# Performance work log

Measured on AMD Instinct MI355X. Metric: run time of the kernel, lower is better.

## Reference

```python
import jax, jax.numpy as jnp
import numpy as np

NUM_USERS = 100000
NUM_ITEMS = 50000
N_NODES = NUM_USERS + NUM_ITEMS
N_EDGES = 3200000
EMB_DIM = 128
N_LAYERS = 3


def setup_inputs() -> dict:
    key = jax.random.key(0)
    ks = jax.random.split(key, 7)
    # nn.init.normal_(std=0.1) embedding init
    user_emb = jax.random.normal(ks[0], (NUM_USERS, EMB_DIM), dtype=jnp.float32) * 0.1
    item_emb = jax.random.normal(ks[1], (NUM_ITEMS, EMB_DIM), dtype=jnp.float32) * 0.1
    # static normalized adjacency in COO form (values from D^-1/2 A D^-1/2 are positive)
    edge_row = jax.random.randint(ks[2], (N_EDGES,), 0, N_NODES, dtype=jnp.int32)
    edge_col = jax.random.randint(ks[3], (N_EDGES,), 0, N_NODES, dtype=jnp.int32)
    edge_val = jax.random.uniform(ks[4], (N_EDGES,), dtype=jnp.float32)
    users = jax.random.randint(ks[5], (2048,), 0, NUM_USERS, dtype=jnp.int32)
    items = jax.random.randint(ks[6], (2048,), 0, NUM_ITEMS, dtype=jnp.int32)
    return {
        "user_emb": user_emb,
        "item_emb": item_emb,
        "edge_val": edge_val,
        "edge_row": edge_row,
        "edge_col": edge_col,
        "users": users,
        "items": items,
    }


def reference(user_emb, item_emb, edge_val, edge_row, edge_col, users, items):
    # computer(): concat user/item tables -> [N, d]
    all_emb = jnp.concatenate([user_emb, item_emb], axis=0)
    acc = all_emb  # running sum of layer embeddings (fused mean over layers)
    emb = all_emb
    for _ in range(N_LAYERS):
        # sparse.mm(G, emb): per-edge gather, scale, scatter-add
        msg = edge_val[:, None] * emb[edge_col]  # [E, d]
        emb = jax.ops.segment_sum(msg, edge_row, num_segments=N_NODES)
        acc = acc + emb
    light_out = acc / jnp.float32(N_LAYERS + 1)  # mean over stacked layer embeddings
    users_emb = light_out[users]
    items_emb = light_out[NUM_USERS + items]
    # gamma = sum(users_emb * items_emb, dim=1)
    return jnp.sum(users_emb * items_emb, axis=1)
```

## Files before the change

kernel.cpp:

```cpp
#include <hip/hip_runtime.h>

#define D 128
#define NUSERS 100000
#define NITEMS 50000
#define NNODES 150000
#define NEDGES 3200000
#define NSEL 2048
#define NBKT 586
#define PBLK 1024
#define EPB (NEDGES / PBLK)
#define MATN (NBKT * PBLK)
#define MB (MATN / 256)
#define BCAP 8192
#define INIT_BLKS 2048
#define FLG_BLKS ((NNODES + 255) / 256)
#define SELSET_BLKS ((2 * NSEL + 255) / 256)
#define COLMASK 0x3FFFFu

typedef unsigned int uint_t;
typedef unsigned short ushort_t;

__device__ inline uint_t bf16_rne(float f) {
    uint_t x = __float_as_uint(f);
    return (x + 0x7FFFu + ((x >> 16) & 1u)) >> 16;
}

__device__ inline int block_excl_scan(int v, int* lds, int nw) {
    int lane = threadIdx.x & 63;
    int wid = (int)(threadIdx.x >> 6);
    int x = v;
    #pragma unroll
    for (int off = 1; off < 64; off <<= 1) {
        int y = __shfl_up(x, off);
        if (lane >= off) x += y;
    }
    if (lane == 63) lds[wid] = x;
    __syncthreads();
    if (wid == 0) {
        int s = (lane < nw) ? lds[lane] : 0;
        #pragma unroll
        for (int off = 1; off < 16; off <<= 1) {
            int y = __shfl_up(s, off);
            if (lane >= off) s += y;
        }
        if (lane < nw) lds[lane] = s;
    }
    __syncthreads();
    int waveoff = (wid == 0) ? 0 : lds[wid - 1];
    return waveoff + x - v;
}

__global__ void k_prologue(const int* __restrict__ row, int* __restrict__ mat,
                           const float4* __restrict__ u4, const float4* __restrict__ i4,
                           uint4* __restrict__ cur,
                           int* __restrict__ flags, int* __restrict__ selflag) {
    __shared__ int h[NBKT];
    int blk = blockIdx.x;
    if (blk < PBLK) {
        for (int i = threadIdx.x; i < NBKT; i += 256) h[i] = 0;
        __syncthreads();
        int beg = blk * EPB, end = beg + EPB;
        for (int e = beg + threadIdx.x; e < end; e += 256)
            atomicAdd(&h[row[e] >> 8], 1);
        __syncthreads();
        for (int i = threadIdx.x; i < NBKT; i += 256)
            mat[i * PBLK + blk] = h[i];
    } else if (blk < PBLK + INIT_BLKS) {
        size_t total8 = (size_t)NNODES * D / 8;
        size_t ub8 = (size_t)NUSERS * D / 8;
        size_t stride = (size_t)INIT_BLKS * 256;
        for (size_t i = (size_t)(blk - PBLK) * 256 + threadIdx.x; i < total8; i += stride) {
            const float4* src = (i < ub8) ? &u4[2 * i] : &i4[2 * (i - ub8)];
            float4 a = src[0], b = src[1];
            uint4 o;
            o.x = (bf16_rne(a.y) << 16) | bf16_rne(a.x);
            o.y = (bf16_rne(a.w) << 16) | bf16_rne(a.z);
            o.z = (bf16_rne(b.y) << 16) | bf16_rne(b.x);
            o.w = (bf16_rne(b.w) << 16) | bf16_rne(b.z);
            cur[i] = o;
        }
    } else {
        int i = (blk - PBLK - INIT_BLKS) * 256 + threadIdx.x;
        if (i < NNODES) { flags[i] = 0; selflag[i] = 0; }
    }
}

__global__ void k_blocksum(const int* __restrict__ src, int* __restrict__ bsums, int n) {
    int i = blockIdx.x * 256 + threadIdx.x;
    int v = (i < n) ? src[i] : 0;
    #pragma unroll
    for (int off = 32; off; off >>= 1) v += __shfl_down(v, off);
    __shared__ int lds[4];
    int lane = threadIdx.x & 63, wid = (int)(threadIdx.x >> 6);
    if (lane == 0) lds[wid] = v;
    __syncthreads();
    if (threadIdx.x == 0) bsums[blockIdx.x] = lds[0] + lds[1] + lds[2] + lds[3];
}

__global__ void k_scan2(int* __restrict__ mat, const int* __restrict__ bsums, int n,
                        const int* __restrict__ users, const int* __restrict__ items,
                        int* __restrict__ selflag, int* __restrict__ flags) {
    int b = blockIdx.x;
    if (b >= MB) {
        int idx = (b - MB) * 256 + threadIdx.x;
        if (idx < 2 * NSEL) {
            int node = (idx < NSEL) ? users[idx] : NUSERS + items[idx - NSEL];
            selflag[node] = 1;
            flags[node] = 1;
        }
        return;
    }
    __shared__ int red[4];
    __shared__ int lds[4];
    int lane = threadIdx.x & 63, wid = (int)(threadIdx.x >> 6);
    int s = 0;
    for (int j = threadIdx.x; j < b; j += 256) s += bsums[j];
    #pragma unroll
    for (int off = 32; off; off >>= 1) s += __shfl_down(s, off);
    if (lane == 0) red[wid] = s;
    __syncthreads();
    int base = red[0] + red[1] + red[2] + red[3];
    int i = b * 256 + threadIdx.x;
    int v = (i < n) ? mat[i] : 0;
    int ex = block_excl_scan(v, lds, 4);
    if (i < n) mat[i] = base + ex;
}

__global__ void k_p2(const int* __restrict__ row, const int* __restrict__ col,
                     const float* __restrict__ val, const int* __restrict__ mat,
                     int2* __restrict__ tmp) {
    __shared__ int cur[NBKT];
    for (int i = threadIdx.x; i < NBKT; i += 256)
        cur[i] = mat[i * PBLK + blockIdx.x];
    __syncthreads();
    int beg = blockIdx.x * EPB, end = beg + EPB;
    for (int e = beg + threadIdx.x; e < end; e += 256) {
        int r = row[e];
        int b = r >> 8;
        int pos = atomicAdd(&cur[b], 1);
        int q = (int)(val[e] * 16384.f + 0.5f);
        if (q > 16383) q = 16383;
        int2 rc;
        rc.x = r & 255;
        rc.y = (int)(((uint_t)q << 18) | (uint_t)col[e]);
        tmp[pos] = rc;
    }
}

__global__ void k_p3(const int2* __restrict__ tmp, const int* __restrict__ mat,
                     uint_t* __restrict__ recs, int* __restrict__ row_start,
                     const int* __restrict__ selflag, int* __restrict__ flags) {
    __shared__ int2 buf[BCAP];
    __shared__ int h[256];
    __shared__ int lds[4];
    __shared__ unsigned char selb[256];
    int b = blockIdx.x;
    int beg = mat[b * PBLK];
    int end = (b + 1 < NBKT) ? mat[(b + 1) * PBLK] : NEDGES;
    int n = end - beg;
    int rowid = b * 256 + threadIdx.x;
    h[threadIdx.x] = 0;
    selb[threadIdx.x] = (rowid < NNODES) ? (unsigned char)selflag[rowid] : 0;
    if (n <= BCAP) {
        for (int i = threadIdx.x; i < n; i += 256) buf[i] = tmp[beg + i];
        __syncthreads();
        for (int i = threadIdx.x; i < n; i += 256)
            atomicAdd(&h[buf[i].x], 1);
        __syncthreads();
        int ex = block_excl_scan(h[threadIdx.x], lds, 4);
        if (rowid < NNODES) row_start[rowid] = beg + ex;
        if (b == NBKT - 1 && threadIdx.x == 0) row_start[NNODES] = NEDGES;
        h[threadIdx.x] = ex;
        __syncthreads();
        for (int i = threadIdx.x; i < n; i += 256) {
            int2 rc = buf[i];
            int r = rc.x;
            int pos = beg + atomicAdd(&h[r], 1);
            recs[pos] = (uint_t)rc.y;
            if (selb[r]) flags[(uint_t)rc.y & COLMASK] = 1;
        }
    } else {
        __syncthreads();
        for (int e = beg + threadIdx.x; e < end; e += 256)
            atomicAdd(&h[tmp[e].x], 1);
        __syncthreads();
        int ex = block_excl_scan(h[threadIdx.x], lds, 4);
        if (rowid < NNODES) row_start[rowid] = beg + ex;
        if (b == NBKT - 1 && threadIdx.x == 0) row_start[NNODES] = NEDGES;
        h[threadIdx.x] = ex;
        __syncthreads();
        for (int e = beg + threadIdx.x; e < end; e += 256) {
            int2 rc = tmp[e];
            int r = rc.x;
            int pos = beg + atomicAdd(&h[r], 1);
            recs[pos] = (uint_t)rc.y;
            if (selb[r]) flags[(uint_t)rc.y & COLMASK] = 1;
        }
    }
}

__global__ void k_spmm_csr(const uint_t* __restrict__ emb, uint_t* __restrict__ outp,
                           const int* __restrict__ row_start,
                           const uint_t* __restrict__ recs,
                           const int* __restrict__ flags, int use_flags) {
    int lane = threadIdx.x & 63;
    int w = (int)((blockIdx.x * blockDim.x + threadIdx.x) >> 6);
    if (w >= NNODES) return;
    if (use_flags && __builtin_amdgcn_readfirstlane(flags[w]) == 0) return;
    int beg = __builtin_amdgcn_readfirstlane(row_start[w]);
    int end = __builtin_amdgcn_readfirstlane(row_start[w + 1]);
    float ax = 0.f, ay = 0.f;
    int e = beg;
    for (; e + 3 < end; e += 4) {
        uint_t q0 = recs[e], q1 = recs[e + 1], q2 = recs[e + 2], q3 = recs[e + 3];
        uint_t g0 = emb[(size_t)(q0 & COLMASK) * 64 + lane];
        uint_t g1 = emb[(size_t)(q1 & COLMASK) * 64 + lane];
        uint_t g2 = emb[(size_t)(q2 & COLMASK) * 64 + lane];
        uint_t g3 = emb[(size_t)(q3 & COLMASK) * 64 + lane];
        float v0 = (float)(q0 >> 18) * (1.f / 16384.f);
        float v1 = (float)(q1 >> 18) * (1.f / 16384.f);
        float v2 = (float)(q2 >> 18) * (1.f / 16384.f);
        float v3 = (float)(q3 >> 18) * (1.f / 16384.f);
        ax += v0 * __uint_as_float(g0 << 16) + v1 * __uint_as_float(g1 << 16)
            + v2 * __uint_as_float(g2 << 16) + v3 * __uint_as_float(g3 << 16);
        ay += v0 * __uint_as_float(g0 & 0xFFFF0000u) + v1 * __uint_as_float(g1 & 0xFFFF0000u)
            + v2 * __uint_as_float(g2 & 0xFFFF0000u) + v3 * __uint_as_float(g3 & 0xFFFF0000u);
    }
    for (; e < end; ++e) {
        uint_t q = recs[e];
        float v = (float)(q >> 18) * (1.f / 16384.f);
        uint_t g = emb[(size_t)(q & COLMASK) * 64 + lane];
        ax += v * __uint_as_float(g << 16);
        ay += v * __uint_as_float(g & 0xFFFF0000u);
    }
    outp[(size_t)w * 64 + lane] = (bf16_rne(ay) << 16) | bf16_rne(ax);
}

__global__ void k_final(const uint_t* __restrict__ embA,
                        const uint_t* __restrict__ embB,
                        const float* __restrict__ user_emb,
                        const float* __restrict__ item_emb,
                        const int* __restrict__ users, const int* __restrict__ items,
                        const int* __restrict__ row_start, const uint_t* __restrict__ recs,
                        float* __restrict__ out) {
    __shared__ float ush[2][64][2];
    int lane = threadIdx.x & 63;
    int wid = (int)(threadIdx.x >> 6);
    int pairIdx = blockIdx.x * 2 + (wid & 1);
    int isItem = wid >> 1;
    int node, idx0;
    const float* e0p;
    if (isItem) {
        idx0 = items[pairIdx];
        node = NUSERS + idx0;
        e0p = &item_emb[(size_t)idx0 * D];
    } else {
        idx0 = users[pairIdx];
        node = idx0;
        e0p = &user_emb[(size_t)idx0 * D];
    }
    const float2 e0 = *(const float2*)(&e0p[lane * 2]);
    uint_t u1 = embB[(size_t)node * 64 + lane];
    uint_t u2 = embA[(size_t)node * 64 + lane];
    float ax = e0.x + __uint_as_float(u1 << 16) + __uint_as_float(u2 << 16);
    float ay = e0.y + __uint_as_float(u1 & 0xFFFF0000u) + __uint_as_float(u2 & 0xFFFF0000u);
    int beg = __builtin_amdgcn_readfirstlane(row_start[node]);
    int end = __builtin_amdgcn_readfirstlane(row_start[node + 1]);
    for (int e = beg; e < end; ++e) {
        uint_t q = recs[e];
        float v = (float)(q >> 18) * (1.f / 16384.f);
        uint_t g = embA[(size_t)(q & COLMASK) * 64 + lane];
        ax += v * __uint_as_float(g << 16);
        ay += v * __uint_as_float(g & 0xFFFF0000u);
    }
    if (!isItem) { ush[wid][lane][0] = ax; ush[wid][lane][1] = ay; }
    __syncthreads();
    if (isItem) {
        float s = ush[wid - 2][lane][0] * ax + ush[wid - 2][lane][1] * ay;
        #pragma unroll
        for (int off = 32; off; off >>= 1) s += __shfl_down(s, off);
        if (lane == 0) out[pairIdx] = s * (1.0f / 16.0f);
    }
}

extern "C" void kernel_launch(void* const* d_in, const int* in_sizes, int n_in,
                              void* d_out, int out_size, void* d_ws, size_t ws_size,
                              hipStream_t stream) {
    const float* user_emb = (const float*)d_in[0];
    const float* item_emb = (const float*)d_in[1];
    const float* edge_val = (const float*)d_in[2];
    const int*   edge_row = (const int*)d_in[3];
    const int*   edge_col = (const int*)d_in[4];
    const int*   users    = (const int*)d_in[5];
    const int*   items    = (const int*)d_in[6];
    float* out = (float*)d_out;

    const size_t tab = (size_t)NNODES * D;
    ushort_t* bufA   = (ushort_t*)d_ws;
    ushort_t* bufB   = bufA + tab;
    uint_t* recs     = (uint_t*)(bufB + tab);
    int2*  tmp       = (int2*)(recs + NEDGES);
    int*   mat       = (int*)(tmp + NEDGES);
    int*   row_start = mat + MATN;
    int*   flags     = row_start + NNODES + 1;
    int*   selflag   = flags + NNODES;
    int*   bsums     = selflag + NNODES;

    k_prologue<<<PBLK + INIT_BLKS + FLG_BLKS, 256, 0, stream>>>(
        edge_row, mat, (const float4*)user_emb, (const float4*)item_emb,
        (uint4*)bufA, flags, selflag);

    k_blocksum<<<MB, 256, 0, stream>>>(mat, bsums, MATN);
    k_scan2<<<MB + SELSET_BLKS, 256, 0, stream>>>(mat, bsums, MATN,
                                                  users, items, selflag, flags);
    k_p2<<<PBLK, 256, 0, stream>>>(edge_row, edge_col, edge_val, mat, tmp);
    k_p3<<<NBKT, 256, 0, stream>>>(tmp, mat, recs, row_start, selflag, flags);

    k_spmm_csr<<<(NNODES + 3) / 4, 256, 0, stream>>>((const uint_t*)bufA, (uint_t*)bufB,
                                                     row_start, recs, flags, 0);
    k_spmm_csr<<<(NNODES + 3) / 4, 256, 0, stream>>>((const uint_t*)bufB, (uint_t*)bufA,
                                                     row_start, recs, flags, 1);
    k_final<<<NSEL / 2, 256, 0, stream>>>((const uint_t*)bufA, (const uint_t*)bufB,
                                          user_emb, item_emb, users, items,
                                          row_start, recs, out);
}
```

Measured before the change: 305.4 us.

## Swizzle block-to-row mapping across XCDs, unroll SpMM gather by 8, defer scaling

Remaps blockIdx in the SpMM kernel so that consecutive rows land on the same XCD, which should improve L2 locality of row_start/recs and output writes. The partition matrix columns are permuted in the same way so the histogram and scatter passes keep XCD-local writes. The SpMM inner loop is unrolled to 8 gathers in flight for more memory-level parallelism. The per-edge dequantization multiply is moved to a single scale at the end. This adds register pressure and relies on the assumed round-robin XCD dispatch order.

```diff
diff --git a/kernel.cpp b/kernel.cpp
--- a/kernel.cpp
+++ b/kernel.cpp
@@ -25,6 +25,14 @@
     return (x + 0x7FFFu + ((x >> 16) & 1u)) >> 16;
 }
 
+__device__ inline int mcol(int b) { return ((b & 7) << 7) | (b >> 3); }
+
+__device__ inline int swz_blk(int b, int n) {
+    int q = n >> 3, r = n & 7;
+    int x = b & 7, i = b >> 3;
+    return (x < r) ? x * (q + 1) + i : r * (q + 1) + (x - r) * q + i;
+}
+
 __device__ inline int block_excl_scan(int v, int* lds, int nw) {
     int lane = threadIdx.x & 63;
     int wid = (int)(threadIdx.x >> 6);
@@ -63,8 +71,9 @@
         for (int e = beg + threadIdx.x; e < end; e += 256)
             atomicAdd(&h[row[e] >> 8], 1);
         __syncthreads();
+        int mb = mcol(blk);
         for (int i = threadIdx.x; i < NBKT; i += 256)
-            mat[i * PBLK + blk] = h[i];
+            mat[i * PBLK + mb] = h[i];
     } else if (blk < PBLK + INIT_BLKS) {
         size_t total8 = (size_t)NNODES * D / 8;
         size_t ub8 = (size_t)NUSERS * D / 8;
@@ -130,8 +139,9 @@
                      const float* __restrict__ val, const int* __restrict__ mat,
                      int2* __restrict__ tmp) {
     __shared__ int cur[NBKT];
+    int mb = mcol(blockIdx.x);
     for (int i = threadIdx.x; i < NBKT; i += 256)
-        cur[i] = mat[i * PBLK + blockIdx.x];
+        cur[i] = mat[i * PBLK + mb];
     __syncthreads();
     int beg = blockIdx.x * EPB, end = beg + EPB;
     for (int e = beg + threadIdx.x; e < end; e += 256) {
@@ -204,23 +214,46 @@
                            const uint_t* __restrict__ recs,
                            const int* __restrict__ flags, int use_flags) {
     int lane = threadIdx.x & 63;
-    int w = (int)((blockIdx.x * blockDim.x + threadIdx.x) >> 6);
+    int blk = swz_blk((int)blockIdx.x, (int)gridDim.x);
+    int w = blk * 4 + (int)(threadIdx.x >> 6);
     if (w >= NNODES) return;
     if (use_flags && __builtin_amdgcn_readfirstlane(flags[w]) == 0) return;
     int beg = __builtin_amdgcn_readfirstlane(row_start[w]);
     int end = __builtin_amdgcn_readfirstlane(row_start[w + 1]);
     float ax = 0.f, ay = 0.f;
     int e = beg;
+    for (; e + 7 < end; e += 8) {
+        uint_t q0 = recs[e],     q1 = recs[e + 1], q2 = recs[e + 2], q3 = recs[e + 3];
+        uint_t q4 = recs[e + 4], q5 = recs[e + 5], q6 = recs[e + 6], q7 = recs[e + 7];
+        uint_t g0 = emb[(size_t)(q0 & COLMASK) * 64 + lane];
+        uint_t g1 = emb[(size_t)(q1 & COLMASK) * 64 + lane];
+        uint_t g2 = emb[(size_t)(q2 & COLMASK) * 64 + lane];
+        uint_t g3 = emb[(size_t)(q3 & COLMASK) * 64 + lane];
+        uint_t g4 = emb[(size_t)(q4 & COLMASK) * 64 + lane];
+        uint_t g5 = emb[(size_t)(q5 & COLMASK) * 64 + lane];
+        uint_t g6 = emb[(size_t)(q6 & COLMASK) * 64 + lane];
+        uint_t g7 = emb[(size_t)(q7 & COLMASK) * 64 + lane];
+        float v0 = (float)(q0 >> 18), v1 = (float)(q1 >> 18);
+        float v2 = (float)(q2 >> 18), v3 = (float)(q3 >> 18);
+        float v4 = (float)(q4 >> 18), v5 = (float)(q5 >> 18);
+        float v6 = (float)(q6 >> 18), v7 = (float)(q7 >> 18);
+        ax += v0 * __uint_as_float(g0 << 16) + v1 * __uint_as_float(g1 << 16)
+            + v2 * __uint_as_float(g2 << 16) + v3 * __uint_as_float(g3 << 16)
+            + v4 * __uint_as_float(g4 << 16) + v5 * __uint_as_float(g5 << 16)
+            + v6 * __uint_as_float(g6 << 16) + v7 * __uint_as_float(g7 << 16);
+        ay += v0 * __uint_as_float(g0 & 0xFFFF0000u) + v1 * __uint_as_float(g1 & 0xFFFF0000u)
+            + v2 * __uint_as_float(g2 & 0xFFFF0000u) + v3 * __uint_as_float(g3 & 0xFFFF0000u)
+            + v4 * __uint_as_float(g4 & 0xFFFF0000u) + v5 * __uint_as_float(g5 & 0xFFFF0000u)
+            + v6 * __uint_as_float(g6 & 0xFFFF0000u) + v7 * __uint_as_float(g7 & 0xFFFF0000u);
+    }
     for (; e + 3 < end; e += 4) {
         uint_t q0 = recs[e], q1 = recs[e + 1], q2 = recs[e + 2], q3 = recs[e + 3];
         uint_t g0 = emb[(size_t)(q0 & COLMASK) * 64 + lane];
         uint_t g1 = emb[(size_t)(q1 & COLMASK) * 64 + lane];
         uint_t g2 = emb[(size_t)(q2 & COLMASK) * 64 + lane];
         uint_t g3 = emb[(size_t)(q3 & COLMASK) * 64 + lane];
-        float v0 = (float)(q0 >> 18) * (1.f / 16384.f);
-        float v1 = (float)(q1 >> 18) * (1.f / 16384.f);
-        float v2 = (float)(q2 >> 18) * (1.f / 16384.f);
-        float v3 = (float)(q3 >> 18) * (1.f / 16384.f);
+        float v0 = (float)(q0 >> 18), v1 = (float)(q1 >> 18);
+        float v2 = (float)(q2 >> 18), v3 = (float)(q3 >> 18);
         ax += v0 * __uint_as_float(g0 << 16) + v1 * __uint_as_float(g1 << 16)
             + v2 * __uint_as_float(g2 << 16) + v3 * __uint_as_float(g3 << 16);
         ay += v0 * __uint_as_float(g0 & 0xFFFF0000u) + v1 * __uint_as_float(g1 & 0xFFFF0000u)
@@ -228,11 +261,13 @@
     }
     for (; e < end; ++e) {
         uint_t q = recs[e];
-        float v = (float)(q >> 18) * (1.f / 16384.f);
+        float v = (float)(q >> 18);
         uint_t g = emb[(size_t)(q & COLMASK) * 64 + lane];
         ax += v * __uint_as_float(g << 16);
         ay += v * __uint_as_float(g & 0xFFFF0000u);
     }
+    ax *= (1.f / 16384.f);
+    ay *= (1.f / 16384.f);
     outp[(size_t)w * 64 + lane] = (bf16_rne(ay) << 16) | bf16_rne(ax);
 }
 
```

Measured after the change: 283.4 us. -7.2%, faster.
